# Performance work log

Hardware: AMD Instinct MI355X
Metric: run time of the kernel (lower is better)

Reference implementation:

```python
import jax, jax.numpy as jnp
import numpy as np

EMBED = 1024
HEADS = 16
HEAD_DIM = EMBED // HEADS
FFN_DIM = 4096
SEQ = 2048
BATCH = 2
EPS = 1e-5


def setup_inputs() -> dict:
    key = jax.random.key(0)
    ks = jax.random.split(key, 13)
    s = lambda n: 1.0 / np.sqrt(n)
    return {
        "x": jax.random.normal(ks[0], (BATCH, SEQ, EMBED), jnp.float32),
        # qkv projection (stored as [in, out])
        "w_qkv": jax.random.normal(ks[1], (EMBED, 3 * EMBED), jnp.float32) * s(EMBED),
        "b_qkv": jax.random.normal(ks[2], (3 * EMBED,), jnp.float32) * 0.02,
        "w_out": jax.random.normal(ks[3], (EMBED, EMBED), jnp.float32) * s(EMBED),
        "b_out": jax.random.normal(ks[4], (EMBED,), jnp.float32) * 0.02,
        # FFN
        "w_up": jax.random.normal(ks[5], (EMBED, FFN_DIM), jnp.float32) * s(EMBED),
        "b_up": jax.random.normal(ks[6], (FFN_DIM,), jnp.float32) * 0.02,
        "w_down": jax.random.normal(ks[7], (FFN_DIM, EMBED), jnp.float32) * s(FFN_DIM),
        "b_down": jax.random.normal(ks[8], (EMBED,), jnp.float32) * 0.02,
        # LayerNorms
        "g1": jnp.ones((EMBED,), jnp.float32),
        "be1": jnp.zeros((EMBED,), jnp.float32),
        "g2": jnp.ones((EMBED,), jnp.float32),
        "be2": jnp.zeros((EMBED,), jnp.float32),
    }


def _layernorm(x, g, b):
    mu = jnp.mean(x, axis=-1, keepdims=True)
    var = jnp.mean(jnp.square(x - mu), axis=-1, keepdims=True)
    return (x - mu) * jax.lax.rsqrt(var + EPS) * g + b


def reference(x, w_qkv, b_qkv, w_out, b_out, w_up, b_up, w_down, b_down, g1, be1, g2, be2):
    B, S, E = x.shape
    qkv = (x @ w_qkv + b_qkv).reshape(B, S, 3, HEADS, HEAD_DIM)
    qkv = jnp.transpose(qkv, (2, 0, 3, 1, 4))
    q, k, v = qkv[0], qkv[1], qkv[2]
    scale = 1.0 / jnp.sqrt(jnp.float32(HEAD_DIM))
    attn = jnp.einsum("bhqd,bhkd->bhqk", q, k) * scale  # [B,H,S,S]
    causal = jnp.tril(jnp.ones((S, S), bool))
    attn = jnp.where(causal, attn, -jnp.inf)
    attn = jax.nn.softmax(attn, axis=-1)
    out = jnp.einsum("bhqk,bhkd->bhqd", attn, v)  # [B,H,S,D]
    out = jnp.transpose(out, (0, 2, 1, 3)).reshape(B, S, E)
    attn_out = out @ w_out + b_out
    x = _layernorm(x + attn_out, g1, be1)
    ffn_out = jax.nn.relu(x @ w_up + b_up) @ w_down + b_down
    return _layernorm(x + ffn_out, g2, be2)
```

## Files before the change

kernel.cpp:

```cpp
#include <hip/hip_runtime.h>
#include <hip/hip_bf16.h>

#define EMBED 1024
#define HEADS 16
#define HDIM 64
#define FFN 4096
#define SEQ 2048
#define BATCH 2
#define MTOT (BATCH*SEQ)
#define QSCALE 0.1803368801111137f

typedef __attribute__((ext_vector_type(8))) short bf16x8;
typedef __attribute__((ext_vector_type(4))) float f32x4;
typedef __attribute__((ext_vector_type(16))) float f32x16;
typedef unsigned short u16;
typedef unsigned int u32;

__device__ __forceinline__ u16 f2bf(float f) {
  union { float f; unsigned u; } v; v.f = f;
  unsigned r = v.u + 0x7FFFu + ((v.u >> 16) & 1u);
  return (u16)(r >> 16);
}

__device__ __forceinline__ void async_ld16(const void* g, void* l) {
  __builtin_amdgcn_global_load_lds((const __attribute__((address_space(1))) void*)g,
                                   (__attribute__((address_space(3))) void*)l,
                                   16, 0, 0);
}

__global__ __launch_bounds__(256) void k_cvt(const float* __restrict__ in,
                                             u16* __restrict__ out, int n4) {
  int i = blockIdx.x * 256 + threadIdx.x;
  int st = gridDim.x * 256;
  for (; i < n4; i += st) {
    float4 v = ((const float4*)in)[i];
    ushort4 o;
    o.x = f2bf(v.x); o.y = f2bf(v.y); o.z = f2bf(v.z); o.w = f2bf(v.w);
    ((ushort4*)out)[i] = o;
  }
}

__global__ __launch_bounds__(256) void k_tr(const float* __restrict__ w,
                                            u16* __restrict__ wT, int K, int N) {
  __shared__ u16 tile[32][33];
  int n0 = blockIdx.x * 32, k0 = blockIdx.y * 32;
  int tx = threadIdx.x, ty = threadIdx.y;
  #pragma unroll
  for (int i = 0; i < 4; ++i) {
    int k = k0 + ty + i * 8;
    tile[ty + i * 8][tx] = f2bf(w[(size_t)k * N + n0 + tx]);
  }
  __syncthreads();
  #pragma unroll
  for (int i = 0; i < 4; ++i) {
    int n = n0 + ty + i * 8;
    wT[(size_t)n * K + k0 + tx] = tile[tx][ty + i * 8];
  }
}

__global__ __launch_bounds__(256) void k_vtr(const u16* __restrict__ V,
                                             u16* __restrict__ Vt) {
  __shared__ u16 t[64][72];
  const int s0 = blockIdx.x * 64;
  const size_t ib = (size_t)blockIdx.y * (size_t)SEQ * HDIM;
  const size_t ob = (size_t)blockIdx.y * (size_t)HDIM * SEQ;
  const int tid = threadIdx.x;
  const int r = tid >> 2, c0 = (tid & 3) * 16;
  bf16x8 v0 = *(const bf16x8*)(V + ib + (size_t)(s0 + r) * HDIM + c0);
  bf16x8 v1 = *(const bf16x8*)(V + ib + (size_t)(s0 + r) * HDIM + c0 + 8);
  #pragma unroll
  for (int j = 0; j < 8; ++j) {
    t[c0 + j][r] = (u16)v0[j];
    t[c0 + 8 + j][r] = (u16)v1[j];
  }
  __syncthreads();
  const int d = tid >> 2, sc = (tid & 3) * 16;
  bf16x8 o0, o1;
  #pragma unroll
  for (int j = 0; j < 8; ++j) { o0[j] = t[d][sc + j]; o1[j] = t[d][sc + 8 + j]; }
  *(bf16x8*)(Vt + ob + (size_t)d * SEQ + s0 + sc) = o0;
  *(bf16x8*)(Vt + ob + (size_t)d * SEQ + s0 + sc + 8) = o1;
}

template <int BN, int BK, int OMODE, bool RELU>
__global__ __launch_bounds__(256) void k_gemm(
    const u16* __restrict__ A, const u16* __restrict__ BT,
    const float* __restrict__ bias,
    void* __restrict__ out0, void* __restrict__ out1, void* __restrict__ out2,
    int M, int N, int K) {
  constexpr int NR = BN / 32;
  constexpr int KS = BK / 32;
  constexpr int TPR = BK / 8;
  constexpr int RPI = 256 / TPR;
  constexpr int CM = TPR - 1;

  __shared__ u16 As[2][128 * BK];
  __shared__ u16 Bs[2][BN * BK];
  const int tid = threadIdx.x;
  const int lane = tid & 63, g = lane >> 4, li = lane & 15;
  const int wid = tid >> 6, wm = wid >> 1, wn = wid & 1;
  const int m0 = blockIdx.y * 128, n0 = blockIdx.x * BN;

  f32x4 acc[4][NR] = {};

  const u16* Ablk = A + (size_t)m0 * K;
  const u16* Bblk = BT + (size_t)n0 * K;
  const int srow = tid / TPR;
  const int scol = ((tid % TPR) ^ (srow & CM)) * 8;

  auto stage = [&](int buf, int kt) {
    #pragma unroll
    for (int r = 0; r < 128; r += RPI)
      async_ld16(Ablk + (size_t)(srow + r) * K + kt + scol, &As[buf][(srow + r) * BK] + (tid % TPR) * 8);
    #pragma unroll
    for (int r = 0; r < BN; r += RPI)
      async_ld16(Bblk + (size_t)(srow + r) * K + kt + scol, &Bs[buf][(srow + r) * BK] + (tid % TPR) * 8);
  };

  stage(0, 0);
  int cur = 0;
  for (int kt = 0; kt < K; kt += BK) {
    __syncthreads();
    if (kt + BK < K) stage(cur ^ 1, kt + BK);

    bf16x8 af[4][KS], bfr[NR][KS];
    #pragma unroll
    for (int i = 0; i < 4; ++i) {
      const int row = wm * 64 + i * 16 + li;
      #pragma unroll
      for (int ks = 0; ks < KS; ++ks) {
        const int c = ks * 4 + g;
        af[i][ks] = *(const bf16x8*)(&As[cur][row * BK] + ((c ^ (row & CM)) & CM) * 8);
      }
    }
    #pragma unroll
    for (int j = 0; j < NR; ++j) {
      const int row = wn * (BN / 2) + j * 16 + li;
      #pragma unroll
      for (int ks = 0; ks < KS; ++ks) {
        const int c = ks * 4 + g;
        bfr[j][ks] = *(const bf16x8*)(&Bs[cur][row * BK] + ((c ^ (row & CM)) & CM) * 8);
      }
    }
    #pragma unroll
    for (int ks = 0; ks < KS; ++ks)
      #pragma unroll
      for (int i = 0; i < 4; ++i)
        #pragma unroll
        for (int j = 0; j < NR; ++j)
          acc[i][j] = __builtin_amdgcn_mfma_f32_16x16x32_bf16(af[i][ks], bfr[j][ks], acc[i][j], 0, 0, 0);
    cur ^= 1;
  }

  float bcol[NR];
  #pragma unroll
  for (int j = 0; j < NR; ++j) bcol[j] = bias[n0 + wn * (BN / 2) + j * 16 + li];

  #pragma unroll
  for (int i = 0; i < 4; ++i) {
    #pragma unroll
    for (int j = 0; j < NR; ++j) {
      #pragma unroll
      for (int r = 0; r < 4; ++r) {
        int row = m0 + wm * 64 + i * 16 + g * 4 + r;
        int col = n0 + wn * (BN / 2) + j * 16 + li;
        float v = acc[i][j][r] + bcol[j];
        if (RELU) v = fmaxf(v, 0.f);
        if (OMODE == 0) {
          ((u16*)out0)[(size_t)row * N + col] = f2bf(v);
        } else if (OMODE == 1) {
          ((float*)out0)[(size_t)row * N + col] = v;
        } else {
          int which = col >> 10, hh = (col >> 6) & 15, d = col & 63;
          int bb = row >> 11, ss = row & 2047;
          if (which == 0) v *= QSCALE;
          u16* dst = which == 0 ? (u16*)out0 : (which == 1 ? (u16*)out1 : (u16*)out2);
          dst[((size_t)((bb * 16 + hh) * 2048 + ss)) * 64 + d] = f2bf(v);
        }
      }
    }
  }
}

__global__ __launch_bounds__(256, 3) void k_attn4(
    const u16* __restrict__ Q, const u16* __restrict__ K,
    const u16* __restrict__ Vt, u16* __restrict__ ctx) {
  const int bh = blockIdx.x;
  const int z  = blockIdx.y;
  const int b = bh >> 4, h = bh & 15;
  const int tid = threadIdx.x;
  const int wid = tid >> 6, lane = tid & 63;
  const int ql = lane & 31, hl = lane >> 5;

  const int s = z * 4 + wid;
  const int t32 = (s & 1) ? (63 - (s >> 1)) : (s >> 1);
  const int wq0 = t32 * 32;
  const int qg = wq0 + ql;

  const size_t kbase = (size_t)bh * SEQ * HDIM;
  const size_t vbase = (size_t)bh * HDIM * SEQ;

  bf16x8 qf[4];
  #pragma unroll
  for (int d4 = 0; d4 < 4; ++d4)
    qf[d4] = *(const bf16x8*)(Q + kbase + (size_t)qg * HDIM + d4 * 16 + hl * 8);

  const u16* kp = K + kbase + (size_t)ql * HDIM + hl * 8;
  const u16* vp = Vt + vbase + (size_t)ql * SEQ + hl * 8;

  f32x16 o0 = {}, o1 = {};
  float m_run = -1e30f, l_run = 0.f;

  const int ntiles = (wq0 + 31) / 64 + 1;
  for (int kt = 0; kt < ntiles; ++kt) {
    const bool kh1 = (kt * 64 + 32 <= wq0 + 31);
    const bool domask = (kt * 64 + (kh1 ? 63 : 31) > wq0);
    const int koff = kt * 64 * HDIM;

    bf16x8 kf0[4], kf1[4];
    #pragma unroll
    for (int d4 = 0; d4 < 4; ++d4) {
      kf0[d4] = *(const bf16x8*)(kp + koff + d4 * 16);
      if (kh1) kf1[d4] = *(const bf16x8*)(kp + koff + 32 * HDIM + d4 * 16);
    }
    bf16x8 vf0[4], vf1[4];
    #pragma unroll
    for (int t = 0; t < 4; ++t)
      if (t < 2 || kh1) {
        vf0[t] = *(const bf16x8*)(vp + kt * 64 + t * 16);
        vf1[t] = *(const bf16x8*)(vp + 32 * SEQ + kt * 64 + t * 16);
      }

    f32x16 S0 = {}, S1 = {};
    #pragma unroll
    for (int d4 = 0; d4 < 4; ++d4)
      S0 = __builtin_amdgcn_mfma_f32_32x32x16_bf16(kf0[d4], qf[d4], S0, 0, 0, 0);
    if (kh1) {
      #pragma unroll
      for (int d4 = 0; d4 < 4; ++d4)
        S1 = __builtin_amdgcn_mfma_f32_32x32x16_bf16(kf1[d4], qf[d4], S1, 0, 0, 0);
    }

    if (domask) {
      const int qrel = qg - kt * 64 - 4 * hl;
      #pragma unroll
      for (int r = 0; r < 16; ++r) {
        const int kc = (r & 3) + 8 * (r >> 2);
        S0[r] = (kc <= qrel) ? S0[r] : -3.0e38f;
      }
      if (kh1) {
        #pragma unroll
        for (int r = 0; r < 16; ++r) {
          const int kc = 32 + (r & 3) + 8 * (r >> 2);
          S1[r] = (kc <= qrel) ? S1[r] : -3.0e38f;
        }
      }
    }

    float mt = -3.0e38f;
    #pragma unroll
    for (int r = 0; r < 16; ++r) mt = fmaxf(mt, S0[r]);
    if (kh1) {
      #pragma unroll
      for (int r = 0; r < 16; ++r) mt = fmaxf(mt, S1[r]);
    }
    mt = fmaxf(mt, __shfl_xor(mt, 32, 64));
    const float mn = fmaxf(m_run, mt);
    const float alpha = exp2f(m_run - mn);
    float sum = 0.f;
    #pragma unroll
    for (int r = 0; r < 16; ++r) { S0[r] = exp2f(S0[r] - mn); sum += S0[r]; }
    if (kh1) {
      #pragma unroll
      for (int r = 0; r < 16; ++r) { S1[r] = exp2f(S1[r] - mn); sum += S1[r]; }
    }
    sum += __shfl_xor(sum, 32, 64);
    l_run = l_run * alpha + sum;
    m_run = mn;
    o0 *= alpha;
    o1 *= alpha;

    u32 pk[2][8], sw[2][8];
    #pragma unroll
    for (int m = 0; m < 4; ++m) {
      asm("v_cvt_pk_bf16_f32 %0, %1, %2" : "=v"(pk[0][2*m])   : "v"(S0[4*m+0]), "v"(S0[4*m+1]));
      asm("v_cvt_pk_bf16_f32 %0, %1, %2" : "=v"(pk[0][2*m+1]) : "v"(S0[4*m+2]), "v"(S0[4*m+3]));
    }
    #pragma unroll
    for (int i = 0; i < 8; ++i) sw[0][i] = __shfl_xor(pk[0][i], 32, 64);
    if (kh1) {
      #pragma unroll
      for (int m = 0; m < 4; ++m) {
        asm("v_cvt_pk_bf16_f32 %0, %1, %2" : "=v"(pk[1][2*m])   : "v"(S1[4*m+0]), "v"(S1[4*m+1]));
        asm("v_cvt_pk_bf16_f32 %0, %1, %2" : "=v"(pk[1][2*m+1]) : "v"(S1[4*m+2]), "v"(S1[4*m+3]));
      }
      #pragma unroll
      for (int i = 0; i < 8; ++i) sw[1][i] = __shfl_xor(pk[1][i], 32, 64);
    }

    #pragma unroll
    for (int t = 0; t < 4; ++t) {
      if (t < 2 || kh1) {
        const int c = t >> 1, m0 = 2 * (t & 1), m1 = m0 + 1;
        union { u32 u[4]; bf16x8 v; } pf;
        pf.u[0] = hl ? sw[c][2*m1]   : pk[c][2*m0];
        pf.u[1] = hl ? sw[c][2*m1+1] : pk[c][2*m0+1];
        pf.u[2] = hl ? pk[c][2*m1]   : sw[c][2*m0];
        pf.u[3] = hl ? pk[c][2*m1+1] : sw[c][2*m0+1];
        o0 = __builtin_amdgcn_mfma_f32_32x32x16_bf16(vf0[t], pf.v, o0, 0, 0, 0);
        o1 = __builtin_amdgcn_mfma_f32_32x32x16_bf16(vf1[t], pf.v, o1, 0, 0, 0);
      }
    }
  }

  const float inv = 1.f / l_run;
  u16* outp = ctx + (size_t)(b * SEQ + qg) * EMBED + h * HDIM + 4 * hl;
  #pragma unroll
  for (int m = 0; m < 4; ++m) {
    ushort4 s0v, s1v;
    s0v.x = f2bf(o0[4*m+0] * inv); s0v.y = f2bf(o0[4*m+1] * inv);
    s0v.z = f2bf(o0[4*m+2] * inv); s0v.w = f2bf(o0[4*m+3] * inv);
    *(ushort4*)(outp + 8 * m) = s0v;
    s1v.x = f2bf(o1[4*m+0] * inv); s1v.y = f2bf(o1[4*m+1] * inv);
    s1v.z = f2bf(o1[4*m+2] * inv); s1v.w = f2bf(o1[4*m+3] * inv);
    *(ushort4*)(outp + 32 + 8 * m) = s1v;
  }
}

__global__ __launch_bounds__(256) void k_add_ln(
    const float* __restrict__ a, const float* __restrict__ bmat,
    const float* __restrict__ gam, const float* __restrict__ bet,
    float* __restrict__ outf, u16* __restrict__ outb) {
  const int row = blockIdx.x;
  const int t = threadIdx.x;
  __shared__ float red[8];
  float4 va = ((const float4*)(a + (size_t)row * EMBED))[t];
  float4 vb = ((const float4*)(bmat + (size_t)row * EMBED))[t];
  float s0 = va.x + vb.x, s1 = va.y + vb.y, s2 = va.z + vb.z, s3 = va.w + vb.w;
  float sum = s0 + s1 + s2 + s3;
  float sq = s0 * s0 + s1 * s1 + s2 * s2 + s3 * s3;
  #pragma unroll
  for (int m = 1; m < 64; m <<= 1) {
    sum += __shfl_xor(sum, m, 64);
    sq += __shfl_xor(sq, m, 64);
  }
  int wid = t >> 6;
  if ((t & 63) == 0) { red[wid] = sum; red[4 + wid] = sq; }
  __syncthreads();
  sum = red[0] + red[1] + red[2] + red[3];
  sq = red[4] + red[5] + red[6] + red[7];
  float mean = sum * (1.f / EMBED);
  float var = sq * (1.f / EMBED) - mean * mean;
  float rstd = rsqrtf(var + 1e-5f);
  float4 gv = ((const float4*)gam)[t], bev = ((const float4*)bet)[t];
  float y0 = (s0 - mean) * rstd * gv.x + bev.x;
  float y1 = (s1 - mean) * rstd * gv.y + bev.y;
  float y2 = (s2 - mean) * rstd * gv.z + bev.z;
  float y3 = (s3 - mean) * rstd * gv.w + bev.w;
  float4 o; o.x = y0; o.y = y1; o.z = y2; o.w = y3;
  ((float4*)(outf + (size_t)row * EMBED))[t] = o;
  if (outb) {
    ushort4 ob; ob.x = f2bf(y0); ob.y = f2bf(y1); ob.z = f2bf(y2); ob.w = f2bf(y3);
    ((ushort4*)(outb + (size_t)row * EMBED))[t] = ob;
  }
}

extern "C" void kernel_launch(void* const* d_in, const int* in_sizes, int n_in,
                              void* d_out, int out_size, void* d_ws, size_t ws_size,
                              hipStream_t stream) {
  const float* x      = (const float*)d_in[0];
  const float* w_qkv  = (const float*)d_in[1];
  const float* b_qkv  = (const float*)d_in[2];
  const float* w_out  = (const float*)d_in[3];
  const float* b_out  = (const float*)d_in[4];
  const float* w_up   = (const float*)d_in[5];
  const float* b_up   = (const float*)d_in[6];
  const float* w_down = (const float*)d_in[7];
  const float* b_down = (const float*)d_in[8];
  const float* g1  = (const float*)d_in[9];
  const float* be1 = (const float*)d_in[10];
  const float* g2  = (const float*)d_in[11];
  const float* be2 = (const float*)d_in[12];

  char* ws = (char*)d_ws;
  size_t off = 0;
  auto alloc = [&](size_t bytes) { void* p = ws + off; off += (bytes + 255) & ~(size_t)255; return p; };

  u16* xb     = (u16*)alloc((size_t)MTOT * EMBED * 2);
  u16* wqkvT  = (u16*)alloc((size_t)3 * EMBED * EMBED * 2);
  u16* woutT  = (u16*)alloc((size_t)EMBED * EMBED * 2);
  u16* wupT   = (u16*)alloc((size_t)FFN * EMBED * 2);
  u16* wdownT = (u16*)alloc((size_t)EMBED * FFN * 2);
  u16* qb     = (u16*)alloc((size_t)MTOT * EMBED * 2);
  u16* kb     = (u16*)alloc((size_t)MTOT * EMBED * 2);
  u16* vb     = (u16*)alloc((size_t)MTOT * EMBED * 2);
  u16* vtb    = (u16*)alloc((size_t)MTOT * EMBED * 2);
  u16* ctx    = (u16*)alloc((size_t)MTOT * EMBED * 2);
  float* attn_proj = (float*)alloc((size_t)MTOT * EMBED * 4);
  float* y_f32     = (float*)alloc((size_t)MTOT * EMBED * 4);
  u16* y_bf16      = (u16*)alloc((size_t)MTOT * EMBED * 2);
  u16* hmid        = (u16*)alloc((size_t)MTOT * FFN * 2);
  float* ffn_o     = (float*)alloc((size_t)MTOT * EMBED * 4);

  dim3 trb(32, 8);
  k_cvt<<<2048, 256, 0, stream>>>(x, xb, MTOT * EMBED / 4);
  k_tr<<<dim3(3 * EMBED / 32, EMBED / 32), trb, 0, stream>>>(w_qkv, wqkvT, EMBED, 3 * EMBED);
  k_tr<<<dim3(EMBED / 32, EMBED / 32), trb, 0, stream>>>(w_out, woutT, EMBED, EMBED);
  k_tr<<<dim3(FFN / 32, EMBED / 32), trb, 0, stream>>>(w_up, wupT, EMBED, FFN);
  k_tr<<<dim3(EMBED / 32, FFN / 32), trb, 0, stream>>>(w_down, wdownT, FFN, EMBED);

  k_gemm<128, 32, 2, false><<<dim3(3 * EMBED / 128, MTOT / 128), 256, 0, stream>>>(
      xb, wqkvT, b_qkv, qb, kb, vb, MTOT, 3 * EMBED, EMBED);

  k_vtr<<<dim3(SEQ / 64, BATCH * HEADS), 256, 0, stream>>>(vb, vtb);

  k_attn4<<<dim3(BATCH * HEADS, 16), 256, 0, stream>>>(qb, kb, vtb, ctx);

  k_gemm<64, 64, 1, false><<<dim3(EMBED / 64, MTOT / 128), 256, 0, stream>>>(
      ctx, woutT, b_out, attn_proj, nullptr, nullptr, MTOT, EMBED, EMBED);

  k_add_ln<<<MTOT, 256, 0, stream>>>(x, attn_proj, g1, be1, y_f32, y_bf16);

  k_gemm<128, 32, 0, true><<<dim3(FFN / 128, MTOT / 128), 256, 0, stream>>>(
      y_bf16, wupT, b_up, hmid, nullptr, nullptr, MTOT, FFN, EMBED);

  k_gemm<64, 64, 1, false><<<dim3(EMBED / 64, MTOT / 128), 256, 0, stream>>>(
      hmid, wdownT, b_down, ffn_o, nullptr, nullptr, MTOT, EMBED, FFN);

  k_add_ln<<<MTOT, 256, 0, stream>>>(y_f32, ffn_o, g2, be2, (float*)d_out, nullptr);

  (void)in_sizes; (void)n_in; (void)out_size; (void)ws_size;
}
```

Before: 280.3 us.

## Split attention KV tiles across wave pairs, lazy rescale, and XCD-swizzle GEMM blocks

The attention kernel now gives each 32-query tile to two waves that take alternating KV tiles, then merges their partial softmax states through shared memory, which doubles the grid and shortens each wave's serial chain. The online softmax skips rescaling the accumulators unless the running max grows by more than a threshold, removing exp and multiply work from most iterations. GEMM block indices are remapped so consecutive workgroups dispatched to the same XCD cover neighbouring tiles, to improve L2 reuse. The cost is extra LDS traffic and a block barrier for the merge, and more resident waves per CU via the raised occupancy bound.

```diff
diff --git a/kernel.cpp b/kernel.cpp
--- a/kernel.cpp
+++ b/kernel.cpp
@@ -99,7 +99,13 @@
   const int tid = threadIdx.x;
   const int lane = tid & 63, g = lane >> 4, li = lane & 15;
   const int wid = tid >> 6, wm = wid >> 1, wn = wid & 1;
-  const int m0 = blockIdx.y * 128, n0 = blockIdx.x * BN;
+
+  const int gx = gridDim.x;
+  const int nwg = gx * gridDim.y;
+  const int flat = blockIdx.y * gx + blockIdx.x;
+  const int cpx = nwg >> 3;
+  const int swz = (flat & 7) * cpx + (flat >> 3);
+  const int m0 = (swz / gx) * 128, n0 = (swz % gx) * BN;
 
   f32x4 acc[4][NR] = {};
 
@@ -182,7 +188,7 @@
   }
 }
 
-__global__ __launch_bounds__(256, 3) void k_attn4(
+__global__ __launch_bounds__(256, 4) void k_attn5(
     const u16* __restrict__ Q, const u16* __restrict__ K,
     const u16* __restrict__ Vt, u16* __restrict__ ctx) {
   const int bh = blockIdx.x;
@@ -190,12 +196,16 @@
   const int b = bh >> 4, h = bh & 15;
   const int tid = threadIdx.x;
   const int wid = tid >> 6, lane = tid & 63;
+  const int pair = wid >> 1, half = wid & 1;
   const int ql = lane & 31, hl = lane >> 5;
 
-  const int s = z * 4 + wid;
+  __shared__ float mrg[2][64][36];
+
+  const int s = z * 2 + pair;
   const int t32 = (s & 1) ? (63 - (s >> 1)) : (s >> 1);
   const int wq0 = t32 * 32;
   const int qg = wq0 + ql;
+  const int nt = ((t32 * 32 + 31) >> 6) + 1;
 
   const size_t kbase = (size_t)bh * SEQ * HDIM;
   const size_t vbase = (size_t)bh * HDIM * SEQ;
@@ -211,8 +221,7 @@
   f32x16 o0 = {}, o1 = {};
   float m_run = -1e30f, l_run = 0.f;
 
-  const int ntiles = (wq0 + 31) / 64 + 1;
-  for (int kt = 0; kt < ntiles; ++kt) {
+  for (int kt = half; kt < nt; kt += 2) {
     const bool kh1 = (kt * 64 + 32 <= wq0 + 31);
     const bool domask = (kt * 64 + (kh1 ? 63 : 31) > wq0);
     const int koff = kt * 64 * HDIM;
@@ -265,20 +274,24 @@
       for (int r = 0; r < 16; ++r) mt = fmaxf(mt, S1[r]);
     }
     mt = fmaxf(mt, __shfl_xor(mt, 32, 64));
-    const float mn = fmaxf(m_run, mt);
-    const float alpha = exp2f(m_run - mn);
+
+    if (!__all(mt <= m_run + 8.0f)) {
+      const float mn = fmaxf(m_run, mt);
+      const float alpha = exp2f(m_run - mn);
+      l_run *= alpha;
+      o0 *= alpha;
+      o1 *= alpha;
+      m_run = mn;
+    }
     float sum = 0.f;
     #pragma unroll
-    for (int r = 0; r < 16; ++r) { S0[r] = exp2f(S0[r] - mn); sum += S0[r]; }
+    for (int r = 0; r < 16; ++r) { S0[r] = exp2f(S0[r] - m_run); sum += S0[r]; }
     if (kh1) {
       #pragma unroll
-      for (int r = 0; r < 16; ++r) { S1[r] = exp2f(S1[r] - mn); sum += S1[r]; }
+      for (int r = 0; r < 16; ++r) { S1[r] = exp2f(S1[r] - m_run); sum += S1[r]; }
     }
     sum += __shfl_xor(sum, 32, 64);
-    l_run = l_run * alpha + sum;
-    m_run = mn;
-    o0 *= alpha;
-    o1 *= alpha;
+    l_run += sum;
 
     u32 pk[2][8], sw[2][8];
     #pragma unroll
@@ -313,16 +326,37 @@
     }
   }
 
-  const float inv = 1.f / l_run;
+  if (half == 1) {
+    float* p = &mrg[pair][lane][0];
+    *(f32x16*)(p) = o0;
+    *(f32x16*)(p + 16) = o1;
+    p[32] = m_run;
+    p[33] = l_run;
+  }
+  __syncthreads();
+  if (half == 1) return;
+
+  const float* p = &mrg[pair][lane][0];
+  f32x16 ob0 = *(const f32x16*)(p);
+  f32x16 ob1 = *(const f32x16*)(p + 16);
+  const float mb = p[32], lb = p[33];
+  const float M = fmaxf(m_run, mb);
+  const float fa = exp2f(m_run - M), fb = exp2f(mb - M);
+  const float inv = 1.f / (l_run * fa + lb * fb);
+
   u16* outp = ctx + (size_t)(b * SEQ + qg) * EMBED + h * HDIM + 4 * hl;
   #pragma unroll
   for (int m = 0; m < 4; ++m) {
     ushort4 s0v, s1v;
-    s0v.x = f2bf(o0[4*m+0] * inv); s0v.y = f2bf(o0[4*m+1] * inv);
-    s0v.z = f2bf(o0[4*m+2] * inv); s0v.w = f2bf(o0[4*m+3] * inv);
+    s0v.x = f2bf((o0[4*m+0] * fa + ob0[4*m+0] * fb) * inv);
+    s0v.y = f2bf((o0[4*m+1] * fa + ob0[4*m+1] * fb) * inv);
+    s0v.z = f2bf((o0[4*m+2] * fa + ob0[4*m+2] * fb) * inv);
+    s0v.w = f2bf((o0[4*m+3] * fa + ob0[4*m+3] * fb) * inv);
     *(ushort4*)(outp + 8 * m) = s0v;
-    s1v.x = f2bf(o1[4*m+0] * inv); s1v.y = f2bf(o1[4*m+1] * inv);
-    s1v.z = f2bf(o1[4*m+2] * inv); s1v.w = f2bf(o1[4*m+3] * inv);
+    s1v.x = f2bf((o1[4*m+0] * fa + ob1[4*m+0] * fb) * inv);
+    s1v.y = f2bf((o1[4*m+1] * fa + ob1[4*m+1] * fb) * inv);
+    s1v.z = f2bf((o1[4*m+2] * fa + ob1[4*m+2] * fb) * inv);
+    s1v.w = f2bf((o1[4*m+3] * fa + ob1[4*m+3] * fb) * inv);
     *(ushort4*)(outp + 32 + 8 * m) = s1v;
   }
 }
@@ -414,7 +448,7 @@
 
   k_vtr<<<dim3(SEQ / 64, BATCH * HEADS), 256, 0, stream>>>(vb, vtb);
 
-  k_attn4<<<dim3(BATCH * HEADS, 16), 256, 0, stream>>>(qb, kb, vtb, ctx);
+  k_attn5<<<dim3(BATCH * HEADS, 32), 256, 0, stream>>>(qb, kb, vtb, ctx);
 
   k_gemm<64, 64, 1, false><<<dim3(EMBED / 64, MTOT / 128), 256, 0, stream>>>(
       ctx, woutT, b_out, attn_proj, nullptr, nullptr, MTOT, EMBED, EMBED);
```

Result: slower. 349.2 us (+24.6%).
